# Kernel optimization log

Measured on AMD Instinct MI355X. Metric: run time of the kernel, lower is better.

Reference implementation:

```python
import jax, jax.numpy as jnp
import numpy as np


def setup_inputs() -> dict:
    key = jax.random.key(0)
    k1, k2, k3, k4 = jax.random.split(key, 4)
    N = 16384          # dispatched token-expert rows (num_tokens * top_k)
    FC1 = 4096         # fc1 intermediate size (gate|up concatenated)
    E = 8              # number of experts
    inp = {
        "input": jax.random.normal(k1, (N, FC1), dtype=jnp.float32),
        "smooth_scale": jax.random.uniform(k2, (E, FC1 // 2), dtype=jnp.float32, minval=0.5, maxval=1.5),
        "sorted_token_ids": jax.random.randint(k3, (N,), 0, N, dtype=jnp.int32),
        "topk_indices": jax.random.randint(k4, (N,), 0, E, dtype=jnp.int32),
        "fc1_intermediate_size": FC1,
    }
    return inp


def reference(input, smooth_scale, sorted_token_ids, topk_indices, fc1_intermediate_size):
    QMAX = 127.0
    x = input.reshape(-1, fc1_intermediate_size)
    d = fc1_intermediate_size // 2
    # MoE dispatch: output row i reads source row sorted_token_ids[i]
    g = x[sorted_token_ids]                         # [N, FC1]
    gate, up = g[:, :d], g[:, d:]                   # [N, d] each
    act = jax.nn.silu(gate) * up                    # fused SwiGLU
    # per-expert smoothing scale selected via topk ids
    act = act * smooth_scale[topk_indices]          # [N, d]
    # per-row dynamic int8 quantization
    amax = jnp.max(jnp.abs(act), axis=-1)           # [N]
    quant_scale = jnp.where(amax > 0, amax / QMAX, jnp.float32(1.0))
    q = jnp.clip(jnp.round(act / quant_scale[:, None]), -QMAX, QMAX)
    quantized_output = q.astype(jnp.int8)
    return (quantized_output, quant_scale)
```

## Files before the change

### kernel.cpp

```cpp
#include <hip/hip_runtime.h>
#include <math.h>


#define THREADS 256

__device__ __forceinline__ float fast_silu(float x) {
    float e = __expf(-x);
    return x * __builtin_amdgcn_rcpf(1.0f + e);
}

template <int D>
__global__ __launch_bounds__(THREADS) void swiglu_moe_quant_kernel(
    const float* __restrict__ input,
    const float* __restrict__ smooth_scale,
    const int*   __restrict__ sorted_token_ids,
    const int*   __restrict__ topk_indices,
    float* __restrict__ q_out,
    float* __restrict__ scale_out)
{
    constexpr int ITERS = D / (THREADS * 4);

    const int row  = blockIdx.x;
    const int tok  = sorted_token_ids[row];
    const int exp_ = topk_indices[row];

    const float* g  = input + (size_t)tok * (size_t)(2 * D);
    const float* up = g + D;
    const float* ss = smooth_scale + (size_t)exp_ * (size_t)D;

    const int t = threadIdx.x;

    float4 act[ITERS];
    float amax = 0.0f;

    #pragma unroll
    for (int k = 0; k < ITERS; ++k) {
        const int j = (t + k * THREADS) * 4;
        float4 gv = *(const float4*)(g  + j);
        float4 uv = *(const float4*)(up + j);
        float4 sv = *(const float4*)(ss + j);
        float4 a;
        a.x = fast_silu(gv.x) * uv.x * sv.x;
        a.y = fast_silu(gv.y) * uv.y * sv.y;
        a.z = fast_silu(gv.z) * uv.z * sv.z;
        a.w = fast_silu(gv.w) * uv.w * sv.w;
        act[k] = a;
        amax = fmaxf(amax, fmaxf(fmaxf(fabsf(a.x), fabsf(a.y)),
                                 fmaxf(fabsf(a.z), fabsf(a.w))));
    }

    #pragma unroll
    for (int off = 32; off > 0; off >>= 1)
        amax = fmaxf(amax, __shfl_down(amax, off));

    __shared__ float wave_max[THREADS / 64];
    const int wave = t >> 6;
    const int lane = t & 63;
    if (lane == 0) wave_max[wave] = amax;
    __syncthreads();
    float m = fmaxf(fmaxf(wave_max[0], wave_max[1]),
                    fmaxf(wave_max[2], wave_max[3]));

    const float qs    = (m > 0.0f) ? (m / 127.0f) : 1.0f;
    const float invqs = 1.0f / qs;
    if (t == 0) scale_out[row] = qs;

    float* qrow = q_out + (size_t)row * (size_t)D;
    #pragma unroll
    for (int k = 0; k < ITERS; ++k) {
        const int j = (t + k * THREADS) * 4;
        float4 a = act[k];
        float4 q;
        q.x = fminf(127.0f, fmaxf(-127.0f, rintf(a.x * invqs)));
        q.y = fminf(127.0f, fmaxf(-127.0f, rintf(a.y * invqs)));
        q.z = fminf(127.0f, fmaxf(-127.0f, rintf(a.z * invqs)));
        q.w = fminf(127.0f, fmaxf(-127.0f, rintf(a.w * invqs)));
        *(float4*)(qrow + j) = q;
    }
}

__global__ __launch_bounds__(THREADS) void swiglu_moe_quant_generic(
    const float* __restrict__ input,
    const float* __restrict__ smooth_scale,
    const int*   __restrict__ sorted_token_ids,
    const int*   __restrict__ topk_indices,
    float* __restrict__ q_out,
    float* __restrict__ scale_out,
    int d)
{
    const int row  = blockIdx.x;
    const int tok  = sorted_token_ids[row];
    const int exp_ = topk_indices[row];
    const float* g  = input + (size_t)tok * (size_t)(2 * d);
    const float* up = g + d;
    const float* ss = smooth_scale + (size_t)exp_ * (size_t)d;
    const int t = threadIdx.x;

    float amax = 0.0f;
    for (int j = t; j < d; j += THREADS) {
        float a = fast_silu(g[j]) * up[j] * ss[j];
        amax = fmaxf(amax, fabsf(a));
    }
    #pragma unroll
    for (int off = 32; off > 0; off >>= 1)
        amax = fmaxf(amax, __shfl_down(amax, off));
    __shared__ float wave_max[THREADS / 64];
    if ((t & 63) == 0) wave_max[t >> 6] = amax;
    __syncthreads();
    float m = fmaxf(fmaxf(wave_max[0], wave_max[1]),
                    fmaxf(wave_max[2], wave_max[3]));
    const float qs    = (m > 0.0f) ? (m / 127.0f) : 1.0f;
    const float invqs = 1.0f / qs;
    if (t == 0) scale_out[row] = qs;
    float* qrow = q_out + (size_t)row * (size_t)d;
    for (int j = t; j < d; j += THREADS) {
        float a = fast_silu(g[j]) * up[j] * ss[j];
        qrow[j] = fminf(127.0f, fmaxf(-127.0f, rintf(a * invqs)));
    }
}

extern "C" void kernel_launch(void* const* d_in, const int* in_sizes, int n_in,
                              void* d_out, int out_size, void* d_ws, size_t ws_size,
                              hipStream_t stream) {
    const float* input        = (const float*)d_in[0];
    const float* smooth_scale = (const float*)d_in[1];
    const int*   sorted_ids   = (const int*)d_in[2];
    const int*   topk_idx     = (const int*)d_in[3];

    const int N   = in_sizes[2];
    const int FC1 = in_sizes[0] / N;
    const int d   = FC1 / 2;

    float* q_out     = (float*)d_out;
    float* scale_out = (float*)d_out + (size_t)N * (size_t)d;

    if (d == 2048) {
        swiglu_moe_quant_kernel<2048><<<N, THREADS, 0, stream>>>(
            input, smooth_scale, sorted_ids, topk_idx, q_out, scale_out);
    } else {
        swiglu_moe_quant_generic<<<N, THREADS, 0, stream>>>(
            input, smooth_scale, sorted_ids, topk_idx, q_out, scale_out, d);
    }
}
```

Measured before the change: 386.6 us.

## Map one row per wavefront and use nontemporal stores for quantized output

```diff
diff --git a/kernel.cpp b/kernel.cpp
--- a/kernel.cpp
+++ b/kernel.cpp
@@ -3,6 +3,8 @@
 
 
 #define THREADS 256
+
+typedef float nfloat4 __attribute__((ext_vector_type(4)));
 
 __device__ __forceinline__ float fast_silu(float x) {
     float e = __expf(-x);
@@ -10,17 +12,22 @@
 }
 
 template <int D>
-__global__ __launch_bounds__(THREADS) void swiglu_moe_quant_kernel(
+__global__ __launch_bounds__(THREADS) void swiglu_moe_quant_wave(
     const float* __restrict__ input,
     const float* __restrict__ smooth_scale,
     const int*   __restrict__ sorted_token_ids,
     const int*   __restrict__ topk_indices,
     float* __restrict__ q_out,
-    float* __restrict__ scale_out)
+    float* __restrict__ scale_out,
+    int N)
 {
-    constexpr int ITERS = D / (THREADS * 4);
+    constexpr int PER = D / (64 * 4);
 
-    const int row  = blockIdx.x;
+    const int wave = threadIdx.x >> 6;
+    const int lane = threadIdx.x & 63;
+    const int row  = blockIdx.x * (THREADS / 64) + wave;
+    if (row >= N) return;
+
     const int tok  = sorted_token_ids[row];
     const int exp_ = topk_indices[row];
 
@@ -28,14 +35,12 @@
     const float* up = g + D;
     const float* ss = smooth_scale + (size_t)exp_ * (size_t)D;
 
-    const int t = threadIdx.x;
-
-    float4 act[ITERS];
+    float4 act[PER];
     float amax = 0.0f;
 
     #pragma unroll
-    for (int k = 0; k < ITERS; ++k) {
-        const int j = (t + k * THREADS) * 4;
+    for (int k = 0; k < PER; ++k) {
+        const int j = (lane + k * 64) * 4;
         float4 gv = *(const float4*)(g  + j);
         float4 uv = *(const float4*)(up + j);
         float4 sv = *(const float4*)(ss + j);
@@ -51,31 +56,23 @@
 
     #pragma unroll
     for (int off = 32; off > 0; off >>= 1)
-        amax = fmaxf(amax, __shfl_down(amax, off));
+        amax = fmaxf(amax, __shfl_xor(amax, off));
 
-    __shared__ float wave_max[THREADS / 64];
-    const int wave = t >> 6;
-    const int lane = t & 63;
-    if (lane == 0) wave_max[wave] = amax;
-    __syncthreads();
-    float m = fmaxf(fmaxf(wave_max[0], wave_max[1]),
-                    fmaxf(wave_max[2], wave_max[3]));
-
-    const float qs    = (m > 0.0f) ? (m / 127.0f) : 1.0f;
+    const float qs    = (amax > 0.0f) ? (amax / 127.0f) : 1.0f;
     const float invqs = 1.0f / qs;
-    if (t == 0) scale_out[row] = qs;
+    if (lane == 0) scale_out[row] = qs;
 
     float* qrow = q_out + (size_t)row * (size_t)D;
     #pragma unroll
-    for (int k = 0; k < ITERS; ++k) {
-        const int j = (t + k * THREADS) * 4;
+    for (int k = 0; k < PER; ++k) {
+        const int j = (lane + k * 64) * 4;
         float4 a = act[k];
-        float4 q;
+        nfloat4 q;
         q.x = fminf(127.0f, fmaxf(-127.0f, rintf(a.x * invqs)));
         q.y = fminf(127.0f, fmaxf(-127.0f, rintf(a.y * invqs)));
         q.z = fminf(127.0f, fmaxf(-127.0f, rintf(a.z * invqs)));
         q.w = fminf(127.0f, fmaxf(-127.0f, rintf(a.w * invqs)));
-        *(float4*)(qrow + j) = q;
+        __builtin_nontemporal_store(q, (nfloat4*)(qrow + j));
     }
 }
 
@@ -135,8 +132,10 @@
     float* scale_out = (float*)d_out + (size_t)N * (size_t)d;
 
     if (d == 2048) {
-        swiglu_moe_quant_kernel<2048><<<N, THREADS, 0, stream>>>(
-            input, smooth_scale, sorted_ids, topk_idx, q_out, scale_out);
+        const int rows_per_block = THREADS / 64;
+        const int blocks = (N + rows_per_block - 1) / rows_per_block;
+        swiglu_moe_quant_wave<2048><<<blocks, THREADS, 0, stream>>>(
+            input, smooth_scale, sorted_ids, topk_idx, q_out, scale_out, N);
     } else {
         swiglu_moe_quant_generic<<<N, THREADS, 0, stream>>>(
             input, smooth_scale, sorted_ids, topk_idx, q_out, scale_out, d);
```

After: 387.1 us. About the same (+0.1%).
